# Performance work log

Hardware: AMD Instinct MI355X
Metric: run time of the kernel (lower is better)

The kernel has to match this reference:

```python
import jax, jax.numpy as jnp
import numpy as np

P, Q = 5, 4
C_IN, C_OUT = 256, 256


def setup_inputs() -> dict:
    key = jax.random.key(0)
    kx, kwp, kbp, kwq = jax.random.split(key, 4)
    x = jax.random.normal(kx, (32, C_IN, 56, 56), dtype=jnp.float32)
    # 1x1 conv weights: convp_i -> Wp[i-1] of shape [O, C]; only convp_1 has bias.
    Wp = jax.random.normal(kwp, (P, C_OUT, C_IN), dtype=jnp.float32) * (1.0 / np.sqrt(C_IN))
    bp = jax.random.normal(kbp, (C_OUT,), dtype=jnp.float32) * 0.01
    Wq = jax.random.normal(kwq, (Q, C_OUT, C_IN), dtype=jnp.float32) * (1.0 / np.sqrt(C_IN))
    return {"x": x, "Wp": Wp, "bp": bp, "Wq": Wq}


def reference(x, Wp, bp, Wq):
    # Build powers x**1 .. x**max(P,Q) via incremental multiply (same math as x**i).
    pmax = max(P, Q)
    pows = [x]
    for _ in range(pmax - 1):
        pows.append(pows[-1] * x)
    Xs = jnp.stack(pows, axis=0)  # [pmax, B, C, H, W]
    # Each 1x1 conv is a pointwise channel-mixing GEMM; sum over orders p/q.
    sum_p = jnp.einsum('pbchw,poc->bohw', Xs[:P], Wp) + bp[None, :, None, None]
    sum_q = jnp.einsum('qbchw,qoc->bohw', Xs[:Q], Wq)
    return sum_p / (1.0 + jnp.abs(sum_q))
```

## Files before the change

### kernel.cpp

```cpp
#include <hip/hip_runtime.h>


typedef __attribute__((ext_vector_type(8))) short bf16x8;
typedef __attribute__((ext_vector_type(8))) unsigned short u16x8;
typedef __attribute__((ext_vector_type(4))) float f32x4;

#define CIN    256
#define HW3    3136
#define MTOT   100352
#define KTOT   1280
#define LDA    40
#define WPLANE (512 * 1280)

__device__ __forceinline__ unsigned short f2bf(float f) {
    union { float f; unsigned int u; } cv; cv.f = f;
    unsigned int u = cv.u;
    return (unsigned short)((u + 0x7FFFu + ((u >> 16) & 1u)) >> 16);
}
__device__ __forceinline__ float bf2f(unsigned short h) {
    union { unsigned int u; float f; } cv; cv.u = ((unsigned int)h) << 16;
    return cv.f;
}

__global__ void pack_w_kernel(const float* __restrict__ Wp,
                              const float* __restrict__ Wq,
                              unsigned short* __restrict__ Whi,
                              unsigned short* __restrict__ Wlo) {
    int idx = blockIdx.x * 256 + threadIdx.x;
    int n = idx / KTOT;
    int k = idx - n * KTOT;
    int p = k >> 8, c = k & 255;
    int o = ((n >> 5) << 4) + (n & 15);
    int isq = (n >> 4) & 1;
    float v;
    if (isq) v = (p < 4) ? Wq[((size_t)p * 256 + o) * 256 + c] : 0.0f;
    else     v = Wp[((size_t)p * 256 + o) * 256 + c];
    unsigned short h = f2bf(v);
    Whi[idx] = h;
    Wlo[idx] = f2bf(v - bf2f(h));
}

__global__ __launch_bounds__(256, 2) void kanv_gemm(
    const float* __restrict__ x,
    const unsigned short* __restrict__ Whi,
    const unsigned short* __restrict__ Wlo,
    const float* __restrict__ bp,
    float* __restrict__ out)
{
    __shared__ unsigned short sAh[128 * LDA];
    __shared__ unsigned short sAl[128 * LDA];
    __shared__ unsigned short sBh[128 * LDA];
    __shared__ unsigned short sBl[128 * LDA];

    const int tid  = threadIdx.x;
    const int lane = tid & 63;
    const int wave = tid >> 6;
    const int wm   = wave >> 1;
    const int wn   = wave & 1;
    const int col  = lane & 15;
    const int quad = lane >> 4;

    const int nt = blockIdx.x & 3;
    const int mt = blockIdx.x >> 2;
    const int m0 = mt * 128;

    const int sm    = tid & 127;
    const int chalf = tid >> 7;
    const int mg  = m0 + sm;
    const int bb  = mg / HW3;
    const int hwl = mg - bb * HW3;
    const float* xbase = x + ((size_t)bb * CIN) * HW3 + hwl;
    const int aoff = sm * LDA + chalf * 16;

    const int nB   = tid >> 1;
    const int kk0B = (tid & 1) * 16;
    const size_t wbase = (size_t)(nt * 128 + nB) * KTOT + kk0B;
    const int boff = nB * LDA + kk0B;

    f32x4 acc[4][4];
#pragma unroll
    for (int mi = 0; mi < 4; ++mi)
#pragma unroll
        for (int ni = 0; ni < 4; ++ni)
            acc[mi][ni] = (f32x4){0.f, 0.f, 0.f, 0.f};

    float xv[16], pw[16];

    for (int g = 0; g < 8; ++g) {
        const float* xp = xbase + (size_t)(g * 32 + chalf * 16) * HW3;
#pragma unroll
        for (int j = 0; j < 16; ++j) xv[j] = xp[(size_t)j * HW3];
#pragma unroll
        for (int j = 0; j < 16; ++j) pw[j] = xv[j];

#pragma unroll
        for (int p = 0; p < 5; ++p) {
            __syncthreads();

            u16x8 h0, h1, l0, l1;
#pragma unroll
            for (int j = 0; j < 8; ++j) {
                unsigned short h = f2bf(pw[j]);
                h0[j] = h; l0[j] = f2bf(pw[j] - bf2f(h));
                h = f2bf(pw[j + 8]);
                h1[j] = h; l1[j] = f2bf(pw[j + 8] - bf2f(h));
            }
            *(u16x8*)&sAh[aoff]     = h0;
            *(u16x8*)&sAh[aoff + 8] = h1;
            *(u16x8*)&sAl[aoff]     = l0;
            *(u16x8*)&sAl[aoff + 8] = l1;

            const size_t wo = wbase + (size_t)(p * 256 + g * 32);
            uint4 wh0 = *(const uint4*)(Whi + wo);
            uint4 wh1 = *(const uint4*)(Whi + wo + 8);
            uint4 wl0 = *(const uint4*)(Wlo + wo);
            uint4 wl1 = *(const uint4*)(Wlo + wo + 8);
            *(uint4*)&sBh[boff]     = wh0;
            *(uint4*)&sBh[boff + 8] = wh1;
            *(uint4*)&sBl[boff]     = wl0;
            *(uint4*)&sBl[boff + 8] = wl1;

            __syncthreads();

            bf16x8 ah[4], al[4], bh[4], bl[4];
#pragma unroll
            for (int mi = 0; mi < 4; ++mi) {
                const int r = (wm * 64 + mi * 16 + col) * LDA + quad * 8;
                ah[mi] = *(const bf16x8*)&sAh[r];
                al[mi] = *(const bf16x8*)&sAl[r];
            }
#pragma unroll
            for (int ni = 0; ni < 4; ++ni) {
                const int r = (wn * 64 + ni * 16 + col) * LDA + quad * 8;
                bh[ni] = *(const bf16x8*)&sBh[r];
                bl[ni] = *(const bf16x8*)&sBl[r];
            }
#pragma unroll
            for (int mi = 0; mi < 4; ++mi)
#pragma unroll
                for (int ni = 0; ni < 4; ++ni) {
                    acc[mi][ni] = __builtin_amdgcn_mfma_f32_16x16x32_bf16(ah[mi], bh[ni], acc[mi][ni], 0, 0, 0);
                    acc[mi][ni] = __builtin_amdgcn_mfma_f32_16x16x32_bf16(al[mi], bh[ni], acc[mi][ni], 0, 0, 0);
                    acc[mi][ni] = __builtin_amdgcn_mfma_f32_16x16x32_bf16(ah[mi], bl[ni], acc[mi][ni], 0, 0, 0);
                }

            if (p < 4) {
#pragma unroll
                for (int j = 0; j < 16; ++j) pw[j] *= xv[j];
            }
        }
    }

#pragma unroll
    for (int j = 0; j < 2; ++j) {
        const int o = (nt * 4 + wn * 2 + j) * 16 + col;
        const float bias = bp[o];
#pragma unroll
        for (int mi = 0; mi < 4; ++mi) {
            f32x4 sp = acc[mi][2 * j];
            f32x4 sq = acc[mi][2 * j + 1];
            const int mrow = m0 + wm * 64 + mi * 16 + quad * 4;
            const int b2  = mrow / HW3;
            const int hw2 = mrow - b2 * HW3;
            float4 v;
            v.x = (sp[0] + bias) / (1.0f + fabsf(sq[0]));
            v.y = (sp[1] + bias) / (1.0f + fabsf(sq[1]));
            v.z = (sp[2] + bias) / (1.0f + fabsf(sq[2]));
            v.w = (sp[3] + bias) / (1.0f + fabsf(sq[3]));
            *(float4*)&out[((size_t)b2 * 256 + o) * HW3 + hw2] = v;
        }
    }
}

extern "C" void kernel_launch(void* const* d_in, const int* in_sizes, int n_in,
                              void* d_out, int out_size, void* d_ws, size_t ws_size,
                              hipStream_t stream) {
    const float* x  = (const float*)d_in[0];
    const float* Wp = (const float*)d_in[1];
    const float* bp = (const float*)d_in[2];
    const float* Wq = (const float*)d_in[3];
    float* out = (float*)d_out;
    unsigned short* Whi = (unsigned short*)d_ws;
    unsigned short* Wlo = Whi + WPLANE;

    pack_w_kernel<<<(WPLANE) / 256, 256, 0, stream>>>(Wp, Wq, Whi, Wlo);
    kanv_gemm<<<(MTOT / 128) * 4, 256, 0, stream>>>(x, Whi, Wlo, bp, out);
}
```

Before: 575.1 us.

## Drop LDS staging: load operands directly into MFMA registers and skip low-order terms

Removes all shared-memory staging and barriers. Each lane loads its MFMA fragments for x straight from global memory and for weights directly from the packed buffers. Activation hi/lo splitting now uses truncation via byte-permute instead of round-to-nearest. The low-order correction MFMAs are skipped for p=0, and the q-columns are skipped at p=4 where their weights are zero. The trade-off is that inter-wave data reuse through LDS is lost, so the same x and weight data is fetched redundantly through the caches, and the truncation slightly alters the numerics.

```diff
diff --git a/kernel.cpp b/kernel.cpp
--- a/kernel.cpp
+++ b/kernel.cpp
@@ -2,14 +2,12 @@
 
 
 typedef __attribute__((ext_vector_type(8))) short bf16x8;
-typedef __attribute__((ext_vector_type(8))) unsigned short u16x8;
 typedef __attribute__((ext_vector_type(4))) float f32x4;
 
 #define CIN    256
 #define HW3    3136
 #define MTOT   100352
 #define KTOT   1280
-#define LDA    40
 #define WPLANE (512 * 1280)
 
 __device__ __forceinline__ unsigned short f2bf(float f) {
@@ -40,6 +38,24 @@
     Wlo[idx] = f2bf(v - bf2f(h));
 }
 
+__device__ __forceinline__ bf16x8 pack_hi8(const float* v) {
+    const unsigned int* u = (const unsigned int*)v;
+    union { unsigned int w[4]; bf16x8 h; } r;
+    r.w[0] = __builtin_amdgcn_perm(u[1], u[0], 0x07060302);
+    r.w[1] = __builtin_amdgcn_perm(u[3], u[2], 0x07060302);
+    r.w[2] = __builtin_amdgcn_perm(u[5], u[4], 0x07060302);
+    r.w[3] = __builtin_amdgcn_perm(u[7], u[6], 0x07060302);
+    return r.h;
+}
+__device__ __forceinline__ void resid8(const float* v, float* l) {
+#pragma unroll
+    for (int j = 0; j < 8; ++j) {
+        union { unsigned int u; float f; } cv;
+        cv.u = ((const unsigned int*)v)[j] & 0xFFFF0000u;
+        l[j] = v[j] - cv.f;
+    }
+}
+
 __global__ __launch_bounds__(256, 2) void kanv_gemm(
     const float* __restrict__ x,
     const unsigned short* __restrict__ Whi,
@@ -47,11 +63,6 @@
     const float* __restrict__ bp,
     float* __restrict__ out)
 {
-    __shared__ unsigned short sAh[128 * LDA];
-    __shared__ unsigned short sAl[128 * LDA];
-    __shared__ unsigned short sBh[128 * LDA];
-    __shared__ unsigned short sBl[128 * LDA];
-
     const int tid  = threadIdx.x;
     const int lane = tid & 63;
     const int wave = tid >> 6;
@@ -62,20 +73,22 @@
 
     const int nt = blockIdx.x & 3;
     const int mt = blockIdx.x >> 2;
-    const int m0 = mt * 128;
+    const int m0 = mt * 128 + wm * 64;
 
-    const int sm    = tid & 127;
-    const int chalf = tid >> 7;
-    const int mg  = m0 + sm;
-    const int bb  = mg / HW3;
-    const int hwl = mg - bb * HW3;
-    const float* xbase = x + ((size_t)bb * CIN) * HW3 + hwl;
-    const int aoff = sm * LDA + chalf * 16;
-
-    const int nB   = tid >> 1;
-    const int kk0B = (tid & 1) * 16;
-    const size_t wbase = (size_t)(nt * 128 + nB) * KTOT + kk0B;
-    const int boff = nB * LDA + kk0B;
+    const float* xb[4];
+#pragma unroll
+    for (int mi = 0; mi < 4; ++mi) {
+        int m  = m0 + mi * 16 + col;
+        int bb = m / HW3, hw = m - bb * HW3;
+        xb[mi] = x + ((size_t)bb * CIN) * HW3 + hw;
+    }
+    const unsigned short *wh[4], *wl[4];
+#pragma unroll
+    for (int ni = 0; ni < 4; ++ni) {
+        int n = nt * 128 + wn * 64 + ni * 16 + col;
+        wh[ni] = Whi + (size_t)n * KTOT + quad * 8;
+        wl[ni] = Wlo + (size_t)n * KTOT + quad * 8;
+    }
 
     f32x4 acc[4][4];
 #pragma unroll
@@ -84,69 +97,50 @@
         for (int ni = 0; ni < 4; ++ni)
             acc[mi][ni] = (f32x4){0.f, 0.f, 0.f, 0.f};
 
-    float xv[16], pw[16];
+    float xv[4][8], pw[4][8];
 
     for (int g = 0; g < 8; ++g) {
-        const float* xp = xbase + (size_t)(g * 32 + chalf * 16) * HW3;
 #pragma unroll
-        for (int j = 0; j < 16; ++j) xv[j] = xp[(size_t)j * HW3];
+        for (int mi = 0; mi < 4; ++mi) {
+            const float* xp = xb[mi] + (size_t)(g * 32 + quad * 8) * HW3;
 #pragma unroll
-        for (int j = 0; j < 16; ++j) pw[j] = xv[j];
+            for (int j = 0; j < 8; ++j) { xv[mi][j] = xp[(size_t)j * HW3]; pw[mi][j] = xv[mi][j]; }
+        }
 
 #pragma unroll
         for (int p = 0; p < 5; ++p) {
-            __syncthreads();
-
-            u16x8 h0, h1, l0, l1;
-#pragma unroll
-            for (int j = 0; j < 8; ++j) {
-                unsigned short h = f2bf(pw[j]);
-                h0[j] = h; l0[j] = f2bf(pw[j] - bf2f(h));
-                h = f2bf(pw[j + 8]);
-                h1[j] = h; l1[j] = f2bf(pw[j + 8] - bf2f(h));
-            }
-            *(u16x8*)&sAh[aoff]     = h0;
-            *(u16x8*)&sAh[aoff + 8] = h1;
-            *(u16x8*)&sAl[aoff]     = l0;
-            *(u16x8*)&sAl[aoff + 8] = l1;
-
-            const size_t wo = wbase + (size_t)(p * 256 + g * 32);
-            uint4 wh0 = *(const uint4*)(Whi + wo);
-            uint4 wh1 = *(const uint4*)(Whi + wo + 8);
-            uint4 wl0 = *(const uint4*)(Wlo + wo);
-            uint4 wl1 = *(const uint4*)(Wlo + wo + 8);
-            *(uint4*)&sBh[boff]     = wh0;
-            *(uint4*)&sBh[boff + 8] = wh1;
-            *(uint4*)&sBl[boff]     = wl0;
-            *(uint4*)&sBl[boff + 8] = wl1;
-
-            __syncthreads();
-
-            bf16x8 ah[4], al[4], bh[4], bl[4];
+            bf16x8 ah[4], al[4];
 #pragma unroll
             for (int mi = 0; mi < 4; ++mi) {
-                const int r = (wm * 64 + mi * 16 + col) * LDA + quad * 8;
-                ah[mi] = *(const bf16x8*)&sAh[r];
-                al[mi] = *(const bf16x8*)&sAl[r];
+                ah[mi] = pack_hi8(pw[mi]);
+                if (p > 0) {
+                    float lo[8];
+                    resid8(pw[mi], lo);
+                    al[mi] = pack_hi8(lo);
+                }
             }
+            const int koff = p * 256 + g * 32;
 #pragma unroll
             for (int ni = 0; ni < 4; ++ni) {
-                const int r = (wn * 64 + ni * 16 + col) * LDA + quad * 8;
-                bh[ni] = *(const bf16x8*)&sBh[r];
-                bl[ni] = *(const bf16x8*)&sBl[r];
+                if (p == 4 && (ni & 1)) continue;
+                bf16x8 bh = *(const bf16x8*)(wh[ni] + koff);
+#pragma unroll
+                for (int mi = 0; mi < 4; ++mi)
+                    acc[mi][ni] = __builtin_amdgcn_mfma_f32_16x16x32_bf16(ah[mi], bh, acc[mi][ni], 0, 0, 0);
+                if (p > 0) {
+                    bf16x8 bl = *(const bf16x8*)(wl[ni] + koff);
+#pragma unroll
+                    for (int mi = 0; mi < 4; ++mi) {
+                        acc[mi][ni] = __builtin_amdgcn_mfma_f32_16x16x32_bf16(al[mi], bh, acc[mi][ni], 0, 0, 0);
+                        acc[mi][ni] = __builtin_amdgcn_mfma_f32_16x16x32_bf16(ah[mi], bl, acc[mi][ni], 0, 0, 0);
+                    }
+                }
             }
-#pragma unroll
-            for (int mi = 0; mi < 4; ++mi)
-#pragma unroll
-                for (int ni = 0; ni < 4; ++ni) {
-                    acc[mi][ni] = __builtin_amdgcn_mfma_f32_16x16x32_bf16(ah[mi], bh[ni], acc[mi][ni], 0, 0, 0);
-                    acc[mi][ni] = __builtin_amdgcn_mfma_f32_16x16x32_bf16(al[mi], bh[ni], acc[mi][ni], 0, 0, 0);
-                    acc[mi][ni] = __builtin_amdgcn_mfma_f32_16x16x32_bf16(ah[mi], bl[ni], acc[mi][ni], 0, 0, 0);
-                }
-
             if (p < 4) {
 #pragma unroll
-                for (int j = 0; j < 16; ++j) pw[j] *= xv[j];
+                for (int mi = 0; mi < 4; ++mi)
+#pragma unroll
+                    for (int j = 0; j < 8; ++j) pw[mi][j] *= xv[mi][j];
             }
         }
     }
@@ -159,7 +153,7 @@
         for (int mi = 0; mi < 4; ++mi) {
             f32x4 sp = acc[mi][2 * j];
             f32x4 sq = acc[mi][2 * j + 1];
-            const int mrow = m0 + wm * 64 + mi * 16 + quad * 4;
+            const int mrow = m0 + mi * 16 + quad * 4;
             const int b2  = mrow / HW3;
             const int hw2 = mrow - b2 * HW3;
             float4 v;
@@ -183,6 +177,6 @@
     unsigned short* Whi = (unsigned short*)d_ws;
     unsigned short* Wlo = Whi + WPLANE;
 
-    pack_w_kernel<<<(WPLANE) / 256, 256, 0, stream>>>(Wp, Wq, Whi, Wlo);
+    pack_w_kernel<<<WPLANE / 256, 256, 0, stream>>>(Wp, Wq, Whi, Wlo);
     kanv_gemm<<<(MTOT / 128) * 4, 256, 0, stream>>>(x, Whi, Wlo, bp, out);
 }
```

Result: slower. 623.3 us (+8.4%).
